# Kernel optimization log

Measured on AMD Instinct MI355X. Metric: run time of the kernel, lower is better.

The kernel has to match this reference:

```python
import jax, jax.numpy as jnp
import numpy as np

B, T, K, H = 8192, 96, 32, 768  # batch, max_len, output_dim (tags), bert hidden


def setup_inputs() -> dict:
    key = jax.random.key(0)
    k1, k2, k3, k4 = jax.random.split(key, 4)
    hidden = jax.random.normal(k1, (B, H), dtype=jnp.float32)
    target = jax.random.randint(k2, (B, T), 0, K, dtype=jnp.int32)
    # Dense(output_dim * max_len) params
    W = jax.random.normal(k3, (H, T * K), dtype=jnp.float32) * 0.02
    b = jnp.zeros((T * K,), dtype=jnp.float32)
    # tf.random.uniform transition matrix
    transitions = jax.random.uniform(k4, (K, K), dtype=jnp.float32)
    return {"hidden": hidden, "target": target, "W": W, "b": b, "transitions": transitions}


def _crf_log_norm(em_tm, transitions):
    # em_tm: [T, B, K] time-major emissions. Forward algorithm (logsumexp recurrence).
    def step(alpha, em_t):
        # alpha: [B, K]; broadcast over next-tag axis
        new = jax.nn.logsumexp(alpha[:, :, None] + transitions[None, :, :], axis=1) + em_t
        return new, None
    alpha, _ = jax.lax.scan(step, em_tm[0], em_tm[1:])
    return jax.nn.logsumexp(alpha, axis=-1)  # [B]


def _crf_sequence_score(em_btk, target, transitions):
    # unary: emission score at gold tags; binary: transition scores along gold path
    unary = jnp.take_along_axis(em_btk, target[..., None], axis=-1)[..., 0].sum(-1)
    binary = transitions[target[:, :-1], target[:, 1:]].sum(-1)
    return unary + binary  # [B]


def _viterbi_decode(em_tm, transitions):
    # em_tm: [T, B, K]. Max-product forward pass collecting backpointers.
    def fwd(v, em_t):
        scores = v[:, :, None] + transitions[None, :, :]  # [B, K_prev, K_next]
        bp = jnp.argmax(scores, axis=1).astype(jnp.int32)  # [B, K]
        return jnp.max(scores, axis=1) + em_t, bp
    v, bps = jax.lax.scan(fwd, em_tm[0], em_tm[1:])  # bps: [T-1, B, K]
    last_tag = jnp.argmax(v, axis=-1).astype(jnp.int32)  # [B]
    # backtrace (reverse scan); output index i is the tag at time i
    def back(tag, bp_t):
        prev = jnp.take_along_axis(bp_t, tag[:, None], axis=1)[:, 0]
        return prev, prev
    _, prevs = jax.lax.scan(back, last_tag, bps, reverse=True)  # [T-1, B]
    tags = jnp.concatenate([prevs, last_tag[None, :]], axis=0)  # [T, B]
    return jnp.transpose(tags), jnp.max(v, axis=-1)


def reference(hidden, target, W, b, transitions):
    # Dense with sigmoid, then reshape to (B, max_len, output_dim)
    em = jax.nn.sigmoid(hidden @ W + b).reshape(hidden.shape[0], T, K)
    em_tm = jnp.transpose(em, (1, 0, 2))  # time-major for scan
    log_likelihood = _crf_sequence_score(em, target, transitions) - _crf_log_norm(em_tm, transitions)
    decode_predict, _ = _viterbi_decode(em_tm, transitions)
    return decode_predict, log_likelihood
```

## Files before the change

kernel.cpp:

```cpp
#include <hip/hip_runtime.h>
#include <cstdint>
#include <cstddef>

#define B_  8192
#define T_  96
#define K_  32
#define H_  768
#define NK_ (T_ * K_)

typedef __attribute__((ext_vector_type(8))) _Float16 f16x8;
typedef __attribute__((ext_vector_type(4))) float    f32x4;
typedef __attribute__((ext_vector_type(2))) float    f32x2;

#define SCALE_UP   4096.0f
#define SCALE_DOWN (1.0f / 16777216.0f)

__device__ __forceinline__ void load_lds16(const void* g, void* l) {
    __builtin_amdgcn_global_load_lds(
        (const __attribute__((address_space(1))) unsigned int*)g,
        (__attribute__((address_space(3))) unsigned int*)l,
        16, 0, 0);
}

__device__ __forceinline__ f32x2 pk_add(f32x2 a, f32x2 b) {
    f32x2 d;
    asm("v_pk_add_f32 %0, %1, %2" : "=v"(d) : "v"(a), "v"(b));
    return d;
}
__device__ __forceinline__ f32x2 pk_fma(f32x2 a, f32x2 b, f32x2 c) {
    f32x2 d;
    asm("v_pk_fma_f32 %0, %1, %2, %3" : "=v"(d) : "v"(a), "v"(b), "v"(c));
    return d;
}

__global__ __launch_bounds__(256) void splitA_kernel(
    const float* __restrict__ A, _Float16* __restrict__ Ath, _Float16* __restrict__ Atl)
{
    const int g   = blockIdx.x * 256 + threadIdx.x;
    const int row = g / 96;
    const int o   = g - row * 96;
    const int ks  = o >> 2, qq = o & 3;
    const int r   = row & 127, rb = row >> 7;
    const size_t dst = (size_t)(rb * 24 + ks) * 4096 + r * 32 + ((qq ^ ((r >> 1) & 3)) << 3);

    f32x4 v0 = *(const f32x4*)(A + (size_t)row * H_ + o * 8);
    f32x4 v1 = *(const f32x4*)(A + (size_t)row * H_ + o * 8 + 4);
    f16x8 hi, lo;
#pragma unroll
    for (int e = 0; e < 8; e++) {
        float x = ((e < 4) ? v0[e] : v1[e - 4]) * SCALE_UP;
        _Float16 h = (_Float16)x;
        hi[e] = h;
        lo[e] = (_Float16)(x - (float)h);
    }
    *(f16x8*)&Ath[dst] = hi;
    *(f16x8*)&Atl[dst] = lo;
}

__global__ __launch_bounds__(256) void splitW_kernel(
    const float* __restrict__ W, _Float16* __restrict__ Wth, _Float16* __restrict__ Wtl)
{
    const int g   = blockIdx.x * 256 + threadIdx.x;
    const int ko  = g / NK_;
    const int col = g - ko * NK_;
    const int k0  = ko * 8;
    const int cb  = col >> 7, n = col & 127;
    const int ks  = k0 >> 5, qq = (k0 & 31) >> 3;
    const size_t dst = (size_t)(cb * 24 + ks) * 4096 + n * 32 + ((qq ^ ((n >> 1) & 3)) << 3);

    f16x8 hi, lo;
#pragma unroll
    for (int j = 0; j < 8; j++) {
        float x = W[(size_t)(k0 + j) * NK_ + col] * SCALE_UP;
        _Float16 h = (_Float16)x;
        hi[j] = h;
        lo[j] = (_Float16)(x - (float)h);
    }
    *(f16x8*)&Wth[dst] = hi;
    *(f16x8*)&Wtl[dst] = lo;
}

__global__ __launch_bounds__(256, 2) void gemm_mfma_sigmoid_kernel(
    const _Float16* __restrict__ Ath, const _Float16* __restrict__ Atl,
    const _Float16* __restrict__ Wth, const _Float16* __restrict__ Wtl,
    const float* __restrict__ bias, float* __restrict__ em)
{
    __shared__ _Float16 lds[2][4][4096];

    const int tid  = threadIdx.x;
    const int cb   = blockIdx.x;
    const int rb   = blockIdx.y;
    const int lane = tid & 63;
    const int w    = tid >> 6;
    const int wr   = w >> 1, wc = w & 1;
    const int fr   = lane & 15;
    const int kg   = lane >> 4;

    const _Float16* srcs[4] = {
        Ath + (size_t)(rb * 24) * 4096, Atl + (size_t)(rb * 24) * 4096,
        Wth + (size_t)(cb * 24) * 4096, Wtl + (size_t)(cb * 24) * 4096 };

    auto stage = [&](int ks, int bb) {
#pragma unroll
        for (int m = 0; m < 4; m++) {
            const _Float16* s = srcs[m] + (size_t)ks * 4096 + w * 1024 + lane * 8;
            _Float16* d = &lds[bb][m][w * 1024];
            load_lds16(s, d);
            load_lds16(s + 512, d + 512);
        }
    };

    f32x4 acc[4][4];
#pragma unroll
    for (int i = 0; i < 4; i++)
#pragma unroll
        for (int j = 0; j < 4; j++) acc[i][j] = (f32x4)0.0f;

    int cur = 0;
    stage(0, 0);

    for (int ks = 0; ks < 24; ks++) {
        __syncthreads();
        if (ks + 1 < 24) stage(ks + 1, cur ^ 1);

        f16x8 fah[4], fal[4], fbh[4], fbl[4];
#pragma unroll
        for (int mi = 0; mi < 4; mi++) {
            const int r   = wr * 64 + mi * 16 + fr;
            const int idx = r * 32 + ((kg ^ ((r >> 1) & 3)) << 3);
            fah[mi] = *(const f16x8*)&lds[cur][0][idx];
            fal[mi] = *(const f16x8*)&lds[cur][1][idx];
        }
#pragma unroll
        for (int ni = 0; ni < 4; ni++) {
            const int r   = wc * 64 + ni * 16 + fr;
            const int idx = r * 32 + ((kg ^ ((r >> 1) & 3)) << 3);
            fbh[ni] = *(const f16x8*)&lds[cur][2][idx];
            fbl[ni] = *(const f16x8*)&lds[cur][3][idx];
        }
#pragma unroll
        for (int mi = 0; mi < 4; mi++)
#pragma unroll
            for (int ni = 0; ni < 4; ni++) {
                acc[mi][ni] = __builtin_amdgcn_mfma_f32_16x16x32_f16(fah[mi], fbh[ni], acc[mi][ni], 0, 0, 0);
                acc[mi][ni] = __builtin_amdgcn_mfma_f32_16x16x32_f16(fah[mi], fbl[ni], acc[mi][ni], 0, 0, 0);
                acc[mi][ni] = __builtin_amdgcn_mfma_f32_16x16x32_f16(fal[mi], fbh[ni], acc[mi][ni], 0, 0, 0);
            }
        cur ^= 1;
    }

    const int er = rb * 128 + wr * 64 + (lane >> 4) * 4;
    const int ec = cb * 128 + wc * 64 + fr;
#pragma unroll
    for (int ni = 0; ni < 4; ni++) {
        const int   gc = ec + ni * 16;
        const float bv = bias[gc];
#pragma unroll
        for (int mi = 0; mi < 4; mi++)
#pragma unroll
            for (int r = 0; r < 4; r++) {
                const int gr = er + mi * 16 + r;
                float x = acc[mi][ni][r] * SCALE_DOWN + bv;
                em[(size_t)gr * NK_ + gc] = 1.0f / (1.0f + __expf(-x));
            }
    }
}

__global__ __launch_bounds__(256) void crf_scan_kernel(
    const float* __restrict__ em,
    const int* __restrict__ target,
    const float* __restrict__ trans,
    float* __restrict__ out_tags,
    float* __restrict__ ll)
{
    __shared__ float  trans_s[K_ * K_];
    __shared__ float  e_s[8][K_];
    __shared__ float  v_s[8][K_];
    __shared__ unsigned int bp_s[8][24][K_];
    __shared__ unsigned char tgt_s[8][T_];

    const int tid = threadIdx.x;
    const int g   = tid >> 5;
    const int k   = tid & 31;
    const int b   = blockIdx.x * 8 + g;

    for (int i = tid; i < K_ * K_; i += 256) trans_s[i] = trans[i];
    __syncthreads();

    f32x2 t2[16], E2[16];
#pragma unroll
    for (int c = 0; c < 16; c++) {
        float a0 = trans_s[(2 * c) * K_ + k];
        float a1 = trans_s[(2 * c + 1) * K_ + k];
        t2[c] = (f32x2){a0, a1};
        E2[c] = (f32x2){__expf(a0), __expf(a1)};
    }

    const float* emb = em + (size_t)b * NK_ + k;

    const int tg0 = target[b * T_ + k];
    const int tg1 = target[b * T_ + 32 + k];
    const int tg2 = target[b * T_ + 64 + k];
    tgt_s[g][k] = (unsigned char)tg0;
    tgt_s[g][k + 32] = (unsigned char)tg1;
    tgt_s[g][k + 64] = (unsigned char)tg2;
    __builtin_amdgcn_wave_barrier();

    const float* emrow = em + (size_t)b * NK_;
    float sc = emrow[k * K_ + tg0] + emrow[(k + 32) * K_ + tg1] + emrow[(k + 64) * K_ + tg2];
    if (k > 0) sc += trans_s[(int)tgt_s[g][k - 1] * K_ + tg0];
    sc += trans_s[(int)tgt_s[g][k + 31] * K_ + tg1];
    sc += trans_s[(int)tgt_s[g][k + 63] * K_ + tg2];

    const float em0 = emb[0];
    float beta = em0;
    float v    = em0;
    float Cr   = 0.0f;
    unsigned int bpw = 0;

    float em_t = emb[1 * K_];

    auto STEP = [&](int t, int sh) {
        float em_n = emb[(t + 1) * K_];
        float e = __expf(beta);
        e_s[g][k] = e;
        v_s[g][k] = v;
        __builtin_amdgcn_wave_barrier();

        f32x2 acc = (f32x2){0.0f, 0.0f};
        float bv = -1e30f;
        int   bi = 0;
#pragma unroll
        for (int q = 0; q < 8; q++) {
            f32x4 eq = *(const f32x4*)&e_s[g][q * 4];
            f32x4 vq = *(const f32x4*)&v_s[g][q * 4];
            acc = pk_fma((f32x2){eq.x, eq.y}, E2[2 * q], acc);
            acc = pk_fma((f32x2){eq.z, eq.w}, E2[2 * q + 1], acc);
            f32x2 svA = pk_add((f32x2){vq.x, vq.y}, t2[2 * q]);
            f32x2 svB = pk_add((f32x2){vq.z, vq.w}, t2[2 * q + 1]);
            {
                float wv = (svA.y > svA.x) ? svA.y : svA.x;
                int   wi = (svA.y > svA.x) ? (4 * q + 1) : (4 * q);
                if (wv > bv) { bv = wv; bi = wi; }
            }
            {
                float wv = (svB.y > svB.x) ? svB.y : svB.x;
                int   wi = (svB.y > svB.x) ? (4 * q + 3) : (4 * q + 2);
                if (wv > bv) { bv = wv; bi = wi; }
            }
        }
        float sum = acc.x + acc.y;
        beta = __logf(sum) + (em_t - 4.0f);
        v    = bv + em_t;
        bpw |= (unsigned int)bi << (8 * sh);
        if (sh == 3) { bp_s[g][(t - 1) >> 2][k] = bpw; bpw = 0; }
        em_t = em_n;
    };

    for (int tb = 1; tb <= 89; tb += 4) {
        STEP(tb, 0); STEP(tb + 1, 1); STEP(tb + 2, 2); STEP(tb + 3, 3);
        if ((tb & 15) == 13) {
            float d = __shfl(beta, 0, 32);
            beta -= d;
            Cr += d;
        }
    }
    STEP(93, 0); STEP(94, 1); STEP(95, 2);
    bp_s[g][23][k] = bpw;
    __builtin_amdgcn_wave_barrier();

    float m2 = beta;
#pragma unroll
    for (int d = 16; d >= 1; d >>= 1) m2 = fmaxf(m2, __shfl_xor(m2, d));
    float s2 = __expf(beta - m2);
#pragma unroll
    for (int d = 16; d >= 1; d >>= 1) s2 += __shfl_xor(s2, d);
    const float logZ = 380.0f + Cr + m2 + __logf(s2);

    float scr = sc;
#pragma unroll
    for (int d = 16; d >= 1; d >>= 1) scr += __shfl_xor(scr, d);

    float bvv = v;
    int   bii = k;
#pragma unroll
    for (int d = 16; d >= 1; d >>= 1) {
        float ov = __shfl_xor(bvv, d);
        int   oi = __shfl_xor(bii, d);
        if (ov > bvv || (ov == bvv && oi < bii)) { bvv = ov; bii = oi; }
    }

    if (k == 0) {
        ll[b] = scr - logZ;
        float* ot = out_tags + (size_t)b * T_;
        int tag = bii;
        ot[T_ - 1] = (float)tag;
        for (int t = T_ - 2; t >= 0; t--) {
            unsigned int wd = bp_s[g][t >> 2][tag];
            tag = (wd >> (8 * (t & 3))) & 0xFF;
            ot[t] = (float)tag;
        }
    }
}

extern "C" void kernel_launch(void* const* d_in, const int* in_sizes, int n_in,
                              void* d_out, int out_size, void* d_ws, size_t ws_size,
                              hipStream_t stream)
{
    const float* hidden = (const float*)d_in[0];
    const int*   target = (const int*)d_in[1];
    const float* W      = (const float*)d_in[2];
    const float* bias   = (const float*)d_in[3];
    const float* trans  = (const float*)d_in[4];

    float* out      = (float*)d_out;
    float* out_tags = out;
    float* out_ll   = out + (size_t)B_ * T_;

    char* ws = (char*)d_ws;
    const size_t emB = (size_t)B_ * NK_ * 4;
    const size_t ahB = (size_t)B_ * H_ * 2;
    const size_t whB = (size_t)H_ * NK_ * 2;
    float*    em  = (float*)ws;
    _Float16* Ath = (_Float16*)(ws + emB);
    _Float16* Atl = (_Float16*)(ws + emB + ahB);
    _Float16* Wth = (_Float16*)(ws + emB + 2 * ahB);
    _Float16* Wtl = (_Float16*)(ws + emB + 2 * ahB + whB);

    splitA_kernel<<<(B_ * 96) / 256, 256, 0, stream>>>(hidden, Ath, Atl);
    splitW_kernel<<<(NK_ * 96) / 256, 256, 0, stream>>>(W, Wth, Wtl);

    dim3 gemm_grid(NK_ / 128, B_ / 128);
    gemm_mfma_sigmoid_kernel<<<gemm_grid, 256, 0, stream>>>(Ath, Atl, Wth, Wtl, bias, em);

    crf_scan_kernel<<<B_ / 8, 256, 0, stream>>>(em, target, trans, out_tags, out_ll);
}
```

Baseline: 271.9 us.

## Split CRF scan into 16-lane-per-sequence forward pass plus separate backtrace kernel

Replaces the 32-lane-per-sequence CRF forward/Viterbi kernel with one that uses 16 lanes per sequence, each handling two tags. Instead of building backpointers in LDS, it stores the per-step Viterbi scores to a workspace history buffer. A new backtrace kernel then recomputes the argmax over the previous tag when walking back. The goal is to halve lanes per sequence and shorten the serial critical path, using periodic exponent renormalisation in place of per-step rescaling. The cost is extra global traffic for the score history (it reuses the workspace region of the fp16 split buffers) and an additional kernel launch.

```diff
diff --git a/kernel.cpp b/kernel.cpp
--- a/kernel.cpp
+++ b/kernel.cpp
@@ -166,11 +166,196 @@
     }
 }
 
-__global__ __launch_bounds__(256) void crf_scan_kernel(
+__global__ __launch_bounds__(256) void crf_scan16_kernel(
     const float* __restrict__ em,
     const int* __restrict__ target,
     const float* __restrict__ trans,
+    float2* __restrict__ vhist,
     float* __restrict__ out_tags,
+    float* __restrict__ ll)
+{
+    __shared__ float trans_s[K_ * K_];
+    __shared__ __align__(16) float2 e2s[16][18];
+    __shared__ __align__(16) float2 v2s[16][18];
+    __shared__ unsigned char tgt_s[16][T_];
+
+    const int tid = threadIdx.x;
+    const int g   = tid >> 4;
+    const int l   = tid & 15;
+    const int b   = blockIdx.x * 16 + g;
+
+    for (int i = tid; i < K_ * K_; i += 256) trans_s[i] = trans[i];
+    __syncthreads();
+
+    f32x2 t2a[16], t2b[16], E2a[16], E2b[16];
+#pragma unroll
+    for (int j = 0; j < 16; j++) {
+        float a0 = trans_s[j * K_ + l];
+        float a1 = trans_s[(j + 16) * K_ + l];
+        float b0 = trans_s[j * K_ + (l + 16)];
+        float b1 = trans_s[(j + 16) * K_ + (l + 16)];
+        t2a[j] = (f32x2){a0, a1};  E2a[j] = (f32x2){__expf(a0), __expf(a1)};
+        t2b[j] = (f32x2){b0, b1};  E2b[j] = (f32x2){__expf(b0), __expf(b1)};
+    }
+
+    const float* emb   = em + (size_t)b * NK_;
+    float2*      vh_b  = vhist + (size_t)b * 16 + l;
+
+    int tg[6];
+#pragma unroll
+    for (int j = 0; j < 6; j++) {
+        tg[j] = target[b * T_ + l + 16 * j];
+        tgt_s[g][l + 16 * j] = (unsigned char)tg[j];
+    }
+    __builtin_amdgcn_wave_barrier();
+    float gold = 0.0f;
+#pragma unroll
+    for (int j = 0; j < 6; j++) {
+        const int t = l + 16 * j;
+        gold += emb[t * K_ + tg[j]];
+        if (t > 0) gold += trans_s[(int)tgt_s[g][t - 1] * K_ + tg[j]];
+    }
+
+    float em_a = emb[l];
+    float em_b = emb[l + 16];
+    float Ea = __expf(em_a), Eb = __expf(em_b);
+    float va = em_a,         vb = em_b;
+    int   expo_sum = 0;
+
+    float na = emb[K_ + l];
+    float nb = emb[K_ + l + 16];
+
+    auto STEP = [&](int t) {
+        const float cem_a = na, cem_b = nb;
+        na = emb[(t + 1) * K_ + l];
+        nb = emb[(t + 1) * K_ + l + 16];
+
+        vh_b[(size_t)(t - 1) * (B_ * 16)] = make_float2(va, vb);
+
+        e2s[g][l] = make_float2(Ea, Eb);
+        v2s[g][l] = make_float2(va, vb);
+        __builtin_amdgcn_wave_barrier();
+
+        f32x2 aa0 = (f32x2){0.0f, 0.0f}, aa1 = aa0, ab0 = aa0, ab1 = aa0;
+        float ma0 = -1e30f, ma1 = -1e30f, mb0 = -1e30f, mb1 = -1e30f;
+#pragma unroll
+        for (int j = 0; j < 8; j++) {
+            f32x4 eq = *(const f32x4*)&e2s[g][2 * j];
+            f32x4 vq = *(const f32x4*)&v2s[g][2 * j];
+            f32x2 e0 = __builtin_shufflevector(eq, eq, 0, 1);
+            f32x2 e1 = __builtin_shufflevector(eq, eq, 2, 3);
+            f32x2 v0 = __builtin_shufflevector(vq, vq, 0, 1);
+            f32x2 v1 = __builtin_shufflevector(vq, vq, 2, 3);
+            aa0 = pk_fma(e0, E2a[2 * j], aa0);
+            aa1 = pk_fma(e1, E2a[2 * j + 1], aa1);
+            ab0 = pk_fma(e0, E2b[2 * j], ab0);
+            ab1 = pk_fma(e1, E2b[2 * j + 1], ab1);
+            f32x2 sa0 = pk_add(v0, t2a[2 * j]);
+            f32x2 sa1 = pk_add(v1, t2a[2 * j + 1]);
+            ma0 = fmaxf(fmaxf(ma0, sa0[0]), sa0[1]);
+            ma1 = fmaxf(fmaxf(ma1, sa1[0]), sa1[1]);
+            f32x2 sb0 = pk_add(v0, t2b[2 * j]);
+            f32x2 sb1 = pk_add(v1, t2b[2 * j + 1]);
+            mb0 = fmaxf(fmaxf(mb0, sb0[0]), sb0[1]);
+            mb1 = fmaxf(fmaxf(mb1, sb1[0]), sb1[1]);
+        }
+        f32x2 sa = pk_add(aa0, aa1);
+        f32x2 sb = pk_add(ab0, ab1);
+        Ea = (sa[0] + sa[1]) * __expf(cem_a - 4.0f);
+        Eb = (sb[0] + sb[1]) * __expf(cem_b - 4.0f);
+        va = fmaxf(ma0, ma1) + cem_a;
+        vb = fmaxf(mb0, mb1) + cem_b;
+        __builtin_amdgcn_wave_barrier();
+    };
+
+    auto RENORM = [&]() {
+        float m = fmaxf(Ea, Eb);
+#pragma unroll
+        for (int d = 8; d >= 1; d >>= 1) m = fmaxf(m, __shfl_xor(m, d));
+        const unsigned int ebits = (__float_as_uint(m) >> 23) & 255u;
+        const float s = __uint_as_float((254u - ebits) << 23);
+        Ea *= s; Eb *= s;
+        expo_sum += (int)ebits - 127;
+    };
+
+    for (int tb = 1; tb <= 81; tb += 8) {
+#pragma unroll
+        for (int i = 0; i < 8; i++) STEP(tb + i);
+        RENORM();
+    }
+#pragma unroll
+    for (int i = 0; i < 7; i++) STEP(89 + i);
+
+    float S = Ea + Eb;
+#pragma unroll
+    for (int d = 8; d >= 1; d >>= 1) S += __shfl_xor(S, d);
+    const float logZ = __logf(S) + 380.0f + (float)expo_sum * 0.69314718055994531f;
+
+    float gsum = gold;
+#pragma unroll
+    for (int d = 8; d >= 1; d >>= 1) gsum += __shfl_xor(gsum, d);
+
+    float bv = va; int bi = l;
+    if (vb > bv) { bv = vb; bi = l + 16; }
+#pragma unroll
+    for (int d = 8; d >= 1; d >>= 1) {
+        float ov = __shfl_xor(bv, d);
+        int   oi = __shfl_xor(bi, d);
+        if (ov > bv || (ov == bv && oi < bi)) { bv = ov; bi = oi; }
+    }
+
+    if (l == 0) {
+        ll[b] = gsum - logZ;
+        out_tags[(size_t)b * T_ + (T_ - 1)] = (float)bi;
+    }
+}
+
+__global__ __launch_bounds__(256) void crf_backtrace_kernel(
+    const float2* __restrict__ vhist,
+    const float* __restrict__ trans,
+    float* __restrict__ out_tags)
+{
+    __shared__ float transT_s[K_ * K_];
+
+    const int tid = threadIdx.x;
+    for (int i = tid; i < K_ * K_; i += 256) {
+        const int c = i >> 5, p = i & 31;
+        transT_s[i] = trans[p * K_ + c];
+    }
+    __syncthreads();
+
+    const int g = tid >> 5;
+    const int p = tid & 31;
+    const int b = blockIdx.x * 8 + g;
+
+    const float* vh = (const float*)vhist;
+    float* ot = out_tags + (size_t)b * T_;
+
+    int tag = (int)ot[T_ - 1];
+
+    const size_t lane_off = (size_t)b * 32 + (p & 15) * 2 + (p >> 4);
+    float cur = vh[(size_t)94 * (B_ * 32) + lane_off];
+
+    for (int t = 94; t >= 0; t--) {
+        float nxt = (t > 0) ? vh[(size_t)(t - 1) * (B_ * 32) + lane_off] : 0.0f;
+
+        float bv = cur + transT_s[tag * K_ + p];
+        int   bi = p;
+#pragma unroll
+        for (int d = 16; d >= 1; d >>= 1) {
+            float ov = __shfl_xor(bv, d);
+            int   oi = __shfl_xor(bi, d);
+            if (ov > bv || (ov == bv && oi < bi)) { bv = ov; bi = oi; }
+        }
+        tag = bi;
+        if (p == 0) ot[t] = (float)tag;
+        cur = nxt;
+    }
+}
+
+__global__ __launch_bounds__(256) void crf_scan_fallback_kernel(
+    const float* __restrict__ em, const int* __restrict__ target,
+    const float* __restrict__ trans, float* __restrict__ out_tags,
     float* __restrict__ ll)
 {
     __shared__ float  trans_s[K_ * K_];
@@ -217,7 +402,6 @@
     float v    = em0;
     float Cr   = 0.0f;
     unsigned int bpw = 0;
-
     float em_t = emb[1 * K_];
 
     auto STEP = [&](int t, int sh) {
@@ -318,14 +502,17 @@
     float* out_ll   = out + (size_t)B_ * T_;
 
     char* ws = (char*)d_ws;
-    const size_t emB = (size_t)B_ * NK_ * 4;
-    const size_t ahB = (size_t)B_ * H_ * 2;
-    const size_t whB = (size_t)H_ * NK_ * 2;
+    const size_t emB    = (size_t)B_ * NK_ * 4;
+    const size_t ahB    = (size_t)B_ * H_ * 2;
+    const size_t whB    = (size_t)H_ * NK_ * 2;
+    const size_t vhistB = (size_t)95 * B_ * 16 * 8;
+
     float*    em  = (float*)ws;
     _Float16* Ath = (_Float16*)(ws + emB);
     _Float16* Atl = (_Float16*)(ws + emB + ahB);
     _Float16* Wth = (_Float16*)(ws + emB + 2 * ahB);
     _Float16* Wtl = (_Float16*)(ws + emB + 2 * ahB + whB);
+    float2*   vhist = (float2*)(ws + emB);
 
     splitA_kernel<<<(B_ * 96) / 256, 256, 0, stream>>>(hidden, Ath, Atl);
     splitW_kernel<<<(NK_ * 96) / 256, 256, 0, stream>>>(W, Wth, Wtl);
@@ -333,5 +520,10 @@
     dim3 gemm_grid(NK_ / 128, B_ / 128);
     gemm_mfma_sigmoid_kernel<<<gemm_grid, 256, 0, stream>>>(Ath, Atl, Wth, Wtl, bias, em);
 
-    crf_scan_kernel<<<B_ / 8, 256, 0, stream>>>(em, target, trans, out_tags, out_ll);
-}
+    if (ws_size >= emB + vhistB) {
+        crf_scan16_kernel<<<B_ / 16, 256, 0, stream>>>(em, target, trans, vhist, out_tags, out_ll);
+        crf_backtrace_kernel<<<B_ / 8, 256, 0, stream>>>(vhist, trans, out_tags);
+    } else {
+        crf_scan_fallback_kernel<<<B_ / 8, 256, 0, stream>>>(em, target, trans, out_tags, out_ll);
+    }
+}
```

Result: slower. 286.6 us (+5.4%).

## Process CRF scan with 16 lanes per sequence and linear-domain forward

Applied to the files above, without the earlier changes.

Each sequence now uses 16 lanes, each handling two tags, so a block covers 16 sequences instead of 8. The forward recurrence keeps exp-domain alpha values directly, which removes the per-step log and exp on alpha, and rescales periodically by power-of-two exponent extraction. Halving the lane count per sequence raises per-thread work and register use (four coefficient arrays) in exchange for better ILP and fewer LDS round trips per element. The recursion chain per step gets longer, and more frequent renormalisation is needed to stay within float range.

```diff
diff --git a/kernel.cpp b/kernel.cpp
--- a/kernel.cpp
+++ b/kernel.cpp
@@ -166,134 +166,170 @@
     }
 }
 
-__global__ __launch_bounds__(256) void crf_scan_kernel(
+__global__ __launch_bounds__(256) void crf_scan16_kernel(
     const float* __restrict__ em,
     const int* __restrict__ target,
     const float* __restrict__ trans,
     float* __restrict__ out_tags,
     float* __restrict__ ll)
 {
-    __shared__ float  trans_s[K_ * K_];
-    __shared__ float  e_s[8][K_];
-    __shared__ float  v_s[8][K_];
-    __shared__ unsigned int bp_s[8][24][K_];
-    __shared__ unsigned char tgt_s[8][T_];
+    __shared__ float trans_s[K_ * K_];
+    __shared__ float es[16][40];
+    __shared__ float vs[16][40];
+    __shared__ unsigned int bp_s[16][24][K_];
+    __shared__ unsigned char tgt_s[16][T_];
 
     const int tid = threadIdx.x;
-    const int g   = tid >> 5;
-    const int k   = tid & 31;
-    const int b   = blockIdx.x * 8 + g;
+    const int g   = tid >> 4;
+    const int l   = tid & 15;
+    const int b   = blockIdx.x * 16 + g;
 
     for (int i = tid; i < K_ * K_; i += 256) trans_s[i] = trans[i];
     __syncthreads();
 
-    f32x2 t2[16], E2[16];
+    f32x2 t2a[16], t2b[16], E2a[16], E2b[16];
 #pragma unroll
     for (int c = 0; c < 16; c++) {
-        float a0 = trans_s[(2 * c) * K_ + k];
-        float a1 = trans_s[(2 * c + 1) * K_ + k];
-        t2[c] = (f32x2){a0, a1};
-        E2[c] = (f32x2){__expf(a0), __expf(a1)};
-    }
-
-    const float* emb = em + (size_t)b * NK_ + k;
-
-    const int tg0 = target[b * T_ + k];
-    const int tg1 = target[b * T_ + 32 + k];
-    const int tg2 = target[b * T_ + 64 + k];
-    tgt_s[g][k] = (unsigned char)tg0;
-    tgt_s[g][k + 32] = (unsigned char)tg1;
-    tgt_s[g][k + 64] = (unsigned char)tg2;
+        float a0 = trans_s[(2 * c) * K_ + l];
+        float a1 = trans_s[(2 * c + 1) * K_ + l];
+        float b0 = trans_s[(2 * c) * K_ + l + 16];
+        float b1 = trans_s[(2 * c + 1) * K_ + l + 16];
+        t2a[c] = (f32x2){a0, a1};  E2a[c] = (f32x2){__expf(a0), __expf(a1)};
+        t2b[c] = (f32x2){b0, b1};  E2b[c] = (f32x2){__expf(b0), __expf(b1)};
+    }
+
+    const float* emb = em + (size_t)b * NK_;
+
+    int tg[6];
+#pragma unroll
+    for (int j = 0; j < 6; j++) {
+        tg[j] = target[b * T_ + l + 16 * j];
+        tgt_s[g][l + 16 * j] = (unsigned char)tg[j];
+    }
     __builtin_amdgcn_wave_barrier();
-
-    const float* emrow = em + (size_t)b * NK_;
-    float sc = emrow[k * K_ + tg0] + emrow[(k + 32) * K_ + tg1] + emrow[(k + 64) * K_ + tg2];
-    if (k > 0) sc += trans_s[(int)tgt_s[g][k - 1] * K_ + tg0];
-    sc += trans_s[(int)tgt_s[g][k + 31] * K_ + tg1];
-    sc += trans_s[(int)tgt_s[g][k + 63] * K_ + tg2];
-
-    const float em0 = emb[0];
-    float beta = em0;
-    float v    = em0;
-    float Cr   = 0.0f;
-    unsigned int bpw = 0;
-
-    float em_t = emb[1 * K_];
+    float gold = 0.0f;
+#pragma unroll
+    for (int j = 0; j < 6; j++) {
+        const int t = l + 16 * j;
+        gold += emb[t * K_ + tg[j]];
+        if (t > 0) gold += trans_s[(int)tgt_s[g][t - 1] * K_ + tg[j]];
+    }
+
+    const float em_a = emb[l];
+    const float em_b = emb[l + 16];
+    float Ea = __expf(em_a), Eb = __expf(em_b);
+    float va = em_a,         vb = em_b;
+    int   expo_sum = 0;
+    unsigned int bpwa = 0, bpwb = 0;
+
+    float na = emb[K_ + l];
+    float nb = emb[K_ + l + 16];
 
     auto STEP = [&](int t, int sh) {
-        float em_n = emb[(t + 1) * K_];
-        float e = __expf(beta);
-        e_s[g][k] = e;
-        v_s[g][k] = v;
+        const float cem_a = na, cem_b = nb;
+        na = emb[(t + 1) * K_ + l];
+        nb = emb[(t + 1) * K_ + l + 16];
+
+        es[g][l] = Ea;  es[g][l + 16] = Eb;
+        vs[g][l] = va;  vs[g][l + 16] = vb;
         __builtin_amdgcn_wave_barrier();
 
-        f32x2 acc = (f32x2){0.0f, 0.0f};
-        float bv = -1e30f;
-        int   bi = 0;
-#pragma unroll
-        for (int q = 0; q < 8; q++) {
-            f32x4 eq = *(const f32x4*)&e_s[g][q * 4];
-            f32x4 vq = *(const f32x4*)&v_s[g][q * 4];
-            acc = pk_fma((f32x2){eq.x, eq.y}, E2[2 * q], acc);
-            acc = pk_fma((f32x2){eq.z, eq.w}, E2[2 * q + 1], acc);
-            f32x2 svA = pk_add((f32x2){vq.x, vq.y}, t2[2 * q]);
-            f32x2 svB = pk_add((f32x2){vq.z, vq.w}, t2[2 * q + 1]);
+        f32x2 aa0 = (f32x2){0.0f, 0.0f}, aa1 = aa0, ab0 = aa0, ab1 = aa0;
+        float bva = -1e30f, bvb = -1e30f;
+        int   bia = 0, bib = 0;
+#pragma unroll
+        for (int j = 0; j < 8; j++) {
+            f32x4 eq = *(const f32x4*)&es[g][4 * j];
+            f32x4 vq = *(const f32x4*)&vs[g][4 * j];
+            f32x2 e0 = (f32x2){eq[0], eq[1]};
+            f32x2 e1 = (f32x2){eq[2], eq[3]};
+            f32x2 v0 = (f32x2){vq[0], vq[1]};
+            f32x2 v1 = (f32x2){vq[2], vq[3]};
+
+            aa0 = pk_fma(e0, E2a[2 * j], aa0);
+            aa1 = pk_fma(e1, E2a[2 * j + 1], aa1);
+            ab0 = pk_fma(e0, E2b[2 * j], ab0);
+            ab1 = pk_fma(e1, E2b[2 * j + 1], ab1);
+
             {
-                float wv = (svA.y > svA.x) ? svA.y : svA.x;
-                int   wi = (svA.y > svA.x) ? (4 * q + 1) : (4 * q);
-                if (wv > bv) { bv = wv; bi = wi; }
+                f32x2 s0 = pk_add(v0, t2a[2 * j]);
+                f32x2 s1 = pk_add(v1, t2a[2 * j + 1]);
+                float w0 = (s0[1] > s0[0]) ? s0[1] : s0[0];
+                int   i0 = (s0[1] > s0[0]) ? (4 * j + 1) : (4 * j);
+                float w1 = (s1[1] > s1[0]) ? s1[1] : s1[0];
+                int   i1 = (s1[1] > s1[0]) ? (4 * j + 3) : (4 * j + 2);
+                if (w1 > w0) { w0 = w1; i0 = i1; }
+                if (w0 > bva) { bva = w0; bia = i0; }
             }
             {
-                float wv = (svB.y > svB.x) ? svB.y : svB.x;
-                int   wi = (svB.y > svB.x) ? (4 * q + 3) : (4 * q + 2);
-                if (wv > bv) { bv = wv; bi = wi; }
+                f32x2 s0 = pk_add(v0, t2b[2 * j]);
+                f32x2 s1 = pk_add(v1, t2b[2 * j + 1]);
+                float w0 = (s0[1] > s0[0]) ? s0[1] : s0[0];
+                int   i0 = (s0[1] > s0[0]) ? (4 * j + 1) : (4 * j);
+                float w1 = (s1[1] > s1[0]) ? s1[1] : s1[0];
+                int   i1 = (s1[1] > s1[0]) ? (4 * j + 3) : (4 * j + 2);
+                if (w1 > w0) { w0 = w1; i0 = i1; }
+                if (w0 > bvb) { bvb = w0; bib = i0; }
             }
         }
-        float sum = acc.x + acc.y;
-        beta = __logf(sum) + (em_t - 4.0f);
-        v    = bv + em_t;
-        bpw |= (unsigned int)bi << (8 * sh);
-        if (sh == 3) { bp_s[g][(t - 1) >> 2][k] = bpw; bpw = 0; }
-        em_t = em_n;
+        f32x2 sa = pk_add(aa0, aa1);
+        f32x2 sb = pk_add(ab0, ab1);
+        Ea = (sa[0] + sa[1]) * __expf(cem_a - 4.0f);
+        Eb = (sb[0] + sb[1]) * __expf(cem_b - 4.0f);
+        va = bva + cem_a;
+        vb = bvb + cem_b;
+
+        bpwa |= (unsigned int)bia << (8 * sh);
+        bpwb |= (unsigned int)bib << (8 * sh);
+        if (sh == 3) {
+            bp_s[g][(t - 1) >> 2][l]      = bpwa;
+            bp_s[g][(t - 1) >> 2][l + 16] = bpwb;
+            bpwa = 0; bpwb = 0;
+        }
+        __builtin_amdgcn_wave_barrier();
+    };
+
+    auto RENORM = [&]() {
+        float m = fmaxf(Ea, Eb);
+#pragma unroll
+        for (int d = 8; d >= 1; d >>= 1) m = fmaxf(m, __shfl_xor(m, d));
+        const unsigned int ebits = (__float_as_uint(m) >> 23) & 255u;
+        const float s = __uint_as_float((254u - ebits) << 23);
+        Ea *= s; Eb *= s;
+        expo_sum += (int)ebits - 127;
     };
 
     for (int tb = 1; tb <= 89; tb += 4) {
         STEP(tb, 0); STEP(tb + 1, 1); STEP(tb + 2, 2); STEP(tb + 3, 3);
-        if ((tb & 15) == 13) {
-            float d = __shfl(beta, 0, 32);
-            beta -= d;
-            Cr += d;
-        }
+        if ((tb & 7) == 5) RENORM();
     }
     STEP(93, 0); STEP(94, 1); STEP(95, 2);
-    bp_s[g][23][k] = bpw;
+    bp_s[g][23][l]      = bpwa;
+    bp_s[g][23][l + 16] = bpwb;
     __builtin_amdgcn_wave_barrier();
 
-    float m2 = beta;
-#pragma unroll
-    for (int d = 16; d >= 1; d >>= 1) m2 = fmaxf(m2, __shfl_xor(m2, d));
-    float s2 = __expf(beta - m2);
-#pragma unroll
-    for (int d = 16; d >= 1; d >>= 1) s2 += __shfl_xor(s2, d);
-    const float logZ = 380.0f + Cr + m2 + __logf(s2);
-
-    float scr = sc;
-#pragma unroll
-    for (int d = 16; d >= 1; d >>= 1) scr += __shfl_xor(scr, d);
-
-    float bvv = v;
-    int   bii = k;
-#pragma unroll
-    for (int d = 16; d >= 1; d >>= 1) {
-        float ov = __shfl_xor(bvv, d);
-        int   oi = __shfl_xor(bii, d);
-        if (ov > bvv || (ov == bvv && oi < bii)) { bvv = ov; bii = oi; }
-    }
-
-    if (k == 0) {
-        ll[b] = scr - logZ;
+    float S = Ea + Eb;
+#pragma unroll
+    for (int d = 8; d >= 1; d >>= 1) S += __shfl_xor(S, d);
+    const float logZ = __logf(S) + 380.0f + (float)expo_sum * 0.69314718055994531f;
+
+    float gsum = gold;
+#pragma unroll
+    for (int d = 8; d >= 1; d >>= 1) gsum += __shfl_xor(gsum, d);
+
+    float bv = va; int bi = l;
+    if (vb > bv) { bv = vb; bi = l + 16; }
+#pragma unroll
+    for (int d = 8; d >= 1; d >>= 1) {
+        float ov = __shfl_xor(bv, d);
+        int   oi = __shfl_xor(bi, d);
+        if (ov > bv || (ov == bv && oi < bi)) { bv = ov; bi = oi; }
+    }
+
+    if (l == 0) {
+        ll[b] = gsum - logZ;
         float* ot = out_tags + (size_t)b * T_;
-        int tag = bii;
+        int tag = bi;
         ot[T_ - 1] = (float)tag;
         for (int t = T_ - 2; t >= 0; t--) {
             unsigned int wd = bp_s[g][t >> 2][tag];
@@ -321,6 +357,7 @@
     const size_t emB = (size_t)B_ * NK_ * 4;
     const size_t ahB = (size_t)B_ * H_ * 2;
     const size_t whB = (size_t)H_ * NK_ * 2;
+
     float*    em  = (float*)ws;
     _Float16* Ath = (_Float16*)(ws + emB);
     _Float16* Atl = (_Float16*)(ws + emB + ahB);
@@ -333,5 +370,5 @@
     dim3 gemm_grid(NK_ / 128, B_ / 128);
     gemm_mfma_sigmoid_kernel<<<gemm_grid, 256, 0, stream>>>(Ath, Atl, Wth, Wtl, bias, em);
 
-    crf_scan_kernel<<<B_ / 8, 256, 0, stream>>>(em, target, trans, out_tags, out_ll);
-}
+    crf_scan16_kernel<<<B_ / 16, 256, 0, stream>>>(em, target, trans, out_tags, out_ll);
+}
```

New measurement: 266.2 us. 1.02x faster.
